# Performance work log

Measured on AMD Instinct MI355X. Metric: run time of the kernel, lower is better.

Reference implementation:

```python
import jax, jax.numpy as jnp
import numpy as np

B, C, H, W = 32, 256, 7, 7
HEADS = 8
DIM_HEAD = 64
INNER = HEADS * DIM_HEAD  # 512
N_ANGLES = 16
KS = 5
GROUPS = 32
EPS = 1e-5


def setup_inputs() -> dict:
    key = jax.random.key(0)
    ks = jax.random.split(key, 16)
    w = lambda k, shp: jax.random.normal(k, shp, jnp.float32) * 0.05
    return {
        'x': jax.random.normal(ks[0], (B, C, H, W), jnp.float32),
        'gn_g': jnp.ones((C,), jnp.float32), 'gn_b': jnp.zeros((C,), jnp.float32),
        'sa_w1': w(ks[1], (C // 8, C)), 'sa_b1': jnp.zeros((C // 8,), jnp.float32),
        'sa_w2': w(ks[2], (C, C // 8)), 'sa_b2': jnp.zeros((C,), jnp.float32),
        'sa_gn_g': jnp.ones((C,), jnp.float32), 'sa_gn_b': jnp.zeros((C,), jnp.float32),
        'ra_gn_g': jnp.ones((C,), jnp.float32), 'ra_gn_b': jnp.zeros((C,), jnp.float32),
        'ra_qkv_w': w(ks[3], (3 * C, C)),
        'ra_proj_w': w(ks[4], (C, C)), 'ra_proj_b': jnp.zeros((C,), jnp.float32),
        'aa_ln_g': jnp.ones((C,), jnp.float32), 'aa_ln_b': jnp.zeros((C,), jnp.float32),
        'aa_qkv_w': w(ks[5], (3 * INNER, C)),
        'aa_relpos': w(ks[6], (2 * 7 - 1, 2 * 7 - 1, HEADS)),
        'aa_out_w': w(ks[7], (C, INNER)), 'aa_out_b': jnp.zeros((C,), jnp.float32),
        'ad_dir_w': w(ks[8], (N_ANGLES, C, C, KS, KS)),
        'ad_ap_w1': w(ks[9], (128, C)), 'ad_ap_b1': jnp.zeros((128,), jnp.float32),
        'ad_ap_w2': w(ks[10], (N_ANGLES, 128)), 'ad_ap_b2': jnp.zeros((N_ANGLES,), jnp.float32),
        'ad_proj_w': w(ks[11], (C, C)), 'ad_proj_b': jnp.zeros((C,), jnp.float32),
        'gate_w': w(ks[12], (4, C)), 'gate_b': jnp.zeros((4,), jnp.float32),
        'proj_w': w(ks[13], (C, C)), 'proj_b': jnp.zeros((C,), jnp.float32),
    }


def _gn(x, g, b):
    Bx, Cx, Hx, Wx = x.shape
    xr = x.reshape(Bx, GROUPS, -1)
    m = xr.mean(-1, keepdims=True)
    v = xr.var(-1, keepdims=True)
    xn = ((xr - m) * jax.lax.rsqrt(v + EPS)).reshape(Bx, Cx, Hx, Wx)
    return xn * g[None, :, None, None] + b[None, :, None, None]


def _c1(x, w, b=None):
    y = jnp.einsum('bchw,oc->bohw', x, w)
    return y if b is None else y + b[None, :, None, None]


def _rot_attn_pass(x, qkv_w):
    Bx, Cx, Hx, Wx = x.shape
    d = Cx // HEADS
    q, k, v = jnp.split(_c1(x, qkv_w), 3, axis=1)
    sh = lambda t: t.reshape(Bx, HEADS, d, Hx * Wx).transpose(0, 1, 3, 2)  # b h n d
    q, k, v = sh(q), sh(k), sh(v)
    a = jax.nn.softmax(jnp.einsum('bhid,bhjd->bhij', q, k) * (d ** -0.5), axis=-1)
    o = jnp.einsum('bhij,bhjd->bhid', a, v)
    return o.transpose(0, 1, 3, 2).reshape(Bx, Cx, Hx, Wx)


def _forward(x, gn_g, gn_b, sa_w1, sa_b1, sa_w2, sa_b2, sa_gn_g, sa_gn_b,
             ra_gn_g, ra_gn_b, ra_qkv_w, ra_proj_w, ra_proj_b,
             aa_ln_g, aa_ln_b, aa_qkv_w, aa_relpos, aa_out_w, aa_out_b,
             ad_dir_w, ad_ap_w1, ad_ap_b1, ad_ap_w2, ad_ap_b2, ad_proj_w, ad_proj_b,
             gate_w, gate_b, proj_w, proj_b):
    normed = _gn(x, gn_g, gn_b)

    # --- SpatialAttention branch ---
    wts = jax.nn.sigmoid(_c1(jax.nn.relu(_c1(normed, sa_w1, sa_b1)), sa_w2, sa_b2))
    spatial = _gn(normed * wts + normed, sa_gn_g, sa_gn_b)

    # --- RotationAwareAttention branch: 4 rot90 passes, max-fused ---
    xr = _gn(normed, ra_gn_g, ra_gn_b)
    r0 = _rot_attn_pass(xr, ra_qkv_w)
    r1 = jnp.rot90(_rot_attn_pass(jnp.rot90(xr, 1, (2, 3)), ra_qkv_w), 3, (2, 3))
    r2 = jnp.rot90(_rot_attn_pass(jnp.rot90(xr, 2, (2, 3)), ra_qkv_w), 2, (2, 3))
    r3 = jnp.rot90(_rot_attn_pass(jnp.rot90(xr, 3, (2, 3)), ra_qkv_w), 1, (2, 3))
    mx = jnp.maximum(jnp.maximum(r0, r1), jnp.maximum(r2, r3))
    rotation = _c1(mx, ra_proj_w, ra_proj_b) + normed

    # --- AngleAwareSelfAttention branch (rel-pos-biased MHSA over 49 tokens) ---
    Nn = H * W
    t = normed.reshape(B, C, Nn).transpose(0, 2, 1)  # [B,N,C]
    mu = t.mean(-1, keepdims=True)
    var = t.var(-1, keepdims=True)
    tn = (t - mu) * jax.lax.rsqrt(var + EPS) * aa_ln_g + aa_ln_b
    q, k, v = jnp.split(jnp.einsum('bnc,oc->bno', tn, aa_qkv_w), 3, axis=-1)
    sh = lambda u: u.reshape(B, Nn, HEADS, DIM_HEAD).transpose(0, 2, 1, 3)
    q, k, v = sh(q), sh(k), sh(v)
    dots = jnp.einsum('bhid,bhjd->bhij', q, k) * (DIM_HEAD ** -0.5)
    idx = jnp.arange(Nn)
    yi, xi = idx // W, idx % W
    dy = yi[None, :] - yi[:, None] + (H - 1)  # offsets into 13x13 table
    dx = xi[None, :] - xi[:, None] + (W - 1)
    bias = aa_relpos[dy, dx].transpose(2, 0, 1)[None]  # [1,heads,N,N]
    attn = jax.nn.softmax(dots + bias, axis=-1)
    o = jnp.einsum('bhij,bhjd->bhid', attn, v).transpose(0, 2, 1, 3).reshape(B, Nn, INNER)
    o = jnp.einsum('bni,oi->bno', o, aa_out_w) + aa_out_b
    angle = o.transpose(0, 2, 1).reshape(B, C, H, W) + normed

    # --- AngleAdaptiveAttention branch: 16 directional 5x5 convs + learned softmax gate ---
    dir_out = jax.lax.conv_general_dilated(
        normed, ad_dir_w.reshape(N_ANGLES * C, C, KS, KS), (1, 1), 'SAME',
        dimension_numbers=('NCHW', 'OIHW', 'NCHW')).reshape(B, N_ANGLES, C, H, W)
    gap = normed.mean((2, 3))  # [B,C]
    h1 = jax.nn.relu(gap @ ad_ap_w1.T + ad_ap_b1)
    aw = jax.nn.softmax(h1 @ ad_ap_w2.T + ad_ap_b2, axis=1)  # [B,16]
    comb = jnp.einsum('bkchw,bk->bchw', dir_out, aw)
    adaptive = _c1(comb, ad_proj_w, ad_proj_b) + normed

    # --- gated fusion ---
    gates = jax.nn.softmax(_c1(x, gate_w, gate_b), axis=1)  # [B,4,H,W]
    fused = (spatial * gates[:, 0:1] + rotation * gates[:, 1:2]
             + angle * gates[:, 2:3] + adaptive * gates[:, 3:4])
    return _c1(fused, proj_w, proj_b) + x


def reference(x, gn_g, gn_b, sa_w1, sa_b1, sa_w2, sa_b2, sa_gn_g, sa_gn_b,
              ra_gn_g, ra_gn_b, ra_qkv_w, ra_proj_w, ra_proj_b,
              aa_ln_g, aa_ln_b, aa_qkv_w, aa_relpos, aa_out_w, aa_out_b,
              ad_dir_w, ad_ap_w1, ad_ap_b1, ad_ap_w2, ad_ap_b2, ad_proj_w, ad_proj_b,
              gate_w, gate_b, proj_w, proj_b):
    return _forward(x, gn_g, gn_b, sa_w1, sa_b1, sa_w2, sa_b2, sa_gn_g, sa_gn_b,
                    ra_gn_g, ra_gn_b, ra_qkv_w, ra_proj_w, ra_proj_b,
                    aa_ln_g, aa_ln_b, aa_qkv_w, aa_relpos, aa_out_w, aa_out_b,
                    ad_dir_w, ad_ap_w1, ad_ap_b1, ad_ap_w2, ad_ap_b2, ad_proj_w, ad_proj_b,
                    gate_w, gate_b, proj_w, proj_b)
```

## Files before the change

kernel.cpp:

```cpp
#include <hip/hip_runtime.h>

#define EPS 1e-5f
typedef unsigned short u16;
typedef unsigned int u32;
typedef float f32x4 __attribute__((ext_vector_type(4)));
typedef short bf16x8 __attribute__((ext_vector_type(8)));
typedef unsigned int u32x2 __attribute__((ext_vector_type(2)));

__device__ __forceinline__ float bf2f(u16 h){
  return __uint_as_float(((u32)h) << 16);
}
__device__ __forceinline__ u16 f2bf(float f){
  u32 u = __float_as_uint(f);
  u += 0x7fffu + ((u >> 16) & 1u);
  return (u16)(u >> 16);
}
__device__ __forceinline__ u32 pk2(float lo, float hi){
  return ((u32)f2bf(hi) << 16) | (u32)f2bf(lo);
}
union BF8 { bf16x8 v; u32 u[4]; };

__global__ __launch_bounds__(256) void k_prep1(
    const float* __restrict__ x, const float* __restrict__ gn_g, const float* __restrict__ gn_b,
    const float* __restrict__ ra_g, const float* __restrict__ ra_b,
    float* __restrict__ normed, float* __restrict__ xr, float* __restrict__ gap)
{
  int ch = blockIdx.x, b = blockIdx.y;
  int c0 = ch * 32;
  __shared__ float xs[1568], ns[1568];
  const float* xb = x + ((size_t)b * 256 + c0) * 49;
  for (int i = threadIdx.x; i < 1568; i += 256) xs[i] = xb[i];
  __syncthreads();
  int wv = threadIdx.x >> 6, lane = threadIdx.x & 63;
  const float* gsrc = xs + wv * 392;
  float* ndst = ns + wv * 392;
  float s = 0.f, ss = 0.f;
  for (int i = lane; i < 392; i += 64){ float v = gsrc[i]; s += v; ss += v * v; }
  for (int off = 32; off; off >>= 1){ s += __shfl_down(s, off); ss += __shfl_down(ss, off); }
  s = __shfl(s, 0); ss = __shfl(ss, 0);
  float m = s / 392.f, rs = rsqrtf(ss / 392.f - m * m + EPS);
  for (int i = lane; i < 392; i += 64){
    int c = c0 + wv * 8 + i / 49;
    ndst[i] = (gsrc[i] - m) * rs * gn_g[c] + gn_b[c];
  }
  __syncthreads();
  float* nb = normed + ((size_t)b * 256 + c0) * 49;
  for (int i = threadIdx.x; i < 1568; i += 256) nb[i] = ns[i];
  if (threadIdx.x < 32){
    float g2 = 0.f; const float* rp = ns + threadIdx.x * 49;
    for (int p = 0; p < 49; p++) g2 += rp[p];
    gap[(size_t)b * 256 + c0 + threadIdx.x] = g2 * (1.f / 49.f);
  }
  s = 0.f; ss = 0.f;
  for (int i = lane; i < 392; i += 64){ float v = ndst[i]; s += v; ss += v * v; }
  for (int off = 32; off; off >>= 1){ s += __shfl_down(s, off); ss += __shfl_down(ss, off); }
  s = __shfl(s, 0); ss = __shfl(ss, 0);
  m = s / 392.f; rs = rsqrtf(ss / 392.f - m * m + EPS);
  float* xrb = xr + ((size_t)b * 256 + c0) * 49;
  for (int i = lane; i < 392; i += 64){
    int c = c0 + wv * 8 + i / 49;
    xrb[wv * 392 + i] = (ndst[i] - m) * rs * ra_g[c] + ra_b[c];
  }
}

__device__ void dev_pos(
    const float* __restrict__ x, const float* __restrict__ normed,
    const float* __restrict__ gate_w, const float* __restrict__ gate_b,
    float* __restrict__ gates_g, float* __restrict__ lnm_g, float* __restrict__ lnr_g,
    int pc, int b, float* sm)
{
  float* gw = sm;
  for (int i = threadIdx.x; i < 1024; i += 256) gw[i] = gate_w[i];
  __syncthreads();
  int wv = threadIdx.x >> 6, lane = threadIdx.x & 63;
  for (int pi = wv; pi < 7; pi += 4){
    int p = pc * 7 + pi;
    const float* nb = normed + (size_t)b * 12544 + p;
    const float* xb = x + (size_t)b * 12544 + p;
    float s = 0.f, ss = 0.f, g0 = 0.f, g1 = 0.f, g2 = 0.f, g3 = 0.f;
    for (int c = lane; c < 256; c += 64){
      float nv = nb[c * 49];
      float xv = xb[c * 49];
      s += nv; ss += nv * nv;
      g0 += xv * gw[c]; g1 += xv * gw[256 + c];
      g2 += xv * gw[512 + c]; g3 += xv * gw[768 + c];
    }
    for (int off = 32; off; off >>= 1){
      s += __shfl_down(s, off); ss += __shfl_down(ss, off);
      g0 += __shfl_down(g0, off); g1 += __shfl_down(g1, off);
      g2 += __shfl_down(g2, off); g3 += __shfl_down(g3, off);
    }
    if (lane == 0){
      float mu = s / 256.f;
      lnm_g[b * 49 + p] = mu;
      lnr_g[b * 49 + p] = rsqrtf(ss / 256.f - mu * mu + EPS);
      g0 += gate_b[0]; g1 += gate_b[1]; g2 += gate_b[2]; g3 += gate_b[3];
      float mx = fmaxf(fmaxf(g0, g1), fmaxf(g2, g3));
      float e0 = __expf(g0 - mx), e1 = __expf(g1 - mx), e2 = __expf(g2 - mx), e3 = __expf(g3 - mx);
      float inv = 1.f / (e0 + e1 + e2 + e3);
      float* gg = gates_g + (size_t)b * 196 + p;
      gg[0] = e0 * inv; gg[49] = e1 * inv; gg[98] = e2 * inv; gg[147] = e3 * inv;
    }
  }
}

__device__ void dev_h1aw(
    const float* __restrict__ normed, const float* __restrict__ sa_w1, const float* __restrict__ sa_b1,
    const float* __restrict__ ap_w1, const float* __restrict__ ap_b1,
    const float* __restrict__ ap_w2, const float* __restrict__ ap_b2,
    const float* __restrict__ gap_g,
    float* __restrict__ h1_g, float* __restrict__ aw_g,
    int xb2, int b, float* sm)
{
  int t = threadIdx.x;
  if (xb2 == 7){
    float* gaps = sm; float* h = sm + 256; float* lg = sm + 384;
    gaps[t] = gap_g[b * 256 + t];
    __syncthreads();
    if (t < 128){
      float s = ap_b1[t];
      const float* wr = ap_w1 + t * 256;
      #pragma unroll 4
      for (int c = 0; c < 256; c++) s += gaps[c] * wr[c];
      h[t] = fmaxf(s, 0.f);
    }
    __syncthreads();
    if (t < 16){
      float s = ap_b2[t];
      const float* wr = ap_w2 + t * 128;
      #pragma unroll 4
      for (int o = 0; o < 128; o++) s += h[o] * wr[o];
      lg[t] = s;
    }
    __syncthreads();
    if (t == 0){
      float mx = -1e30f;
      for (int k = 0; k < 16; k++) mx = fmaxf(mx, lg[k]);
      float e[16], smm = 0.f;
      for (int k = 0; k < 16; k++){ e[k] = __expf(lg[k] - mx); smm += e[k]; }
      float inv = 1.f / smm;
      for (int k = 0; k < 16; k++) aw_g[b * 16 + k] = e[k] * inv;
    }
    return;
  }
  float* w1t = sm;
  float* ns2 = sm + 8448;
  int p0 = xb2 * 7;
  for (int i = t; i < 8192; i += 256){
    int o = i >> 8, c = i & 255;
    w1t[c * 33 + o] = sa_w1[i];
  }
  for (int i = t; i < 1792; i += 256){
    int c = i / 7, pl = i - c * 7;
    ns2[i] = normed[(size_t)b * 12544 + c * 49 + p0 + pl];
  }
  __syncthreads();
  if (t < 224){
    int pl = t >> 5, o = t & 31;
    float s = sa_b1[o];
    #pragma unroll 8
    for (int c = 0; c < 256; c++) s += ns2[c * 7 + pl] * w1t[c * 33 + o];
    h1_g[(size_t)b * 1568 + (p0 + pl) * 32 + o] = fmaxf(s, 0.f);
  }
}

__global__ __launch_bounds__(256) void k_pre2(
    const float* __restrict__ x, const float* __restrict__ normed,
    const float* __restrict__ gate_w, const float* __restrict__ gate_b,
    const float* __restrict__ sa_w1, const float* __restrict__ sa_b1,
    const float* __restrict__ ap_w1, const float* __restrict__ ap_b1,
    const float* __restrict__ ap_w2, const float* __restrict__ ap_b2,
    const float* __restrict__ gap_g,
    float* __restrict__ gates_g, float* __restrict__ lnm_g, float* __restrict__ lnr_g,
    float* __restrict__ h1_g, float* __restrict__ aw_g)
{
  __shared__ float sm[10240];
  int bx = blockIdx.x, b = blockIdx.y;
  if (bx < 7)
    dev_pos(x, normed, gate_w, gate_b, gates_g, lnm_g, lnr_g, bx, b, sm);
  else
    dev_h1aw(normed, sa_w1, sa_b1, ap_w1, ap_b1, ap_w2, ap_b2, gap_g, h1_g, aw_g, bx - 7, b, sm);
}

__device__ void dev_spatial(
    const float* __restrict__ normed, const float* __restrict__ h1_g,
    const float* __restrict__ sa_w2, const float* __restrict__ sa_b2,
    const float* __restrict__ sa_g, const float* __restrict__ sa_bb,
    float* __restrict__ spat_g, int gc, int b, float* sm)
{
  float* h1s = sm;
  float* w2s = sm + 1617;
  int t = threadIdx.x;
  for (int i = t; i < 1568; i += 256){
    int p = i >> 5, o = i & 31;
    h1s[p * 33 + o] = h1_g[(size_t)b * 1568 + i];
  }
  for (int i = t; i < 1024; i += 256) w2s[i] = sa_w2[gc * 1024 + i];
  __syncthreads();
  int wv = t >> 6, lane = t & 63;
  int cg0 = wv * 8;
  const float* nb = normed + (size_t)b * 12544 + (gc * 32 + cg0) * 49;
  float tmp[7];
  float s = 0.f, ss = 0.f;
  #pragma unroll
  for (int j = 0; j < 7; j++){
    int i = lane + 64 * j;
    float v = 0.f;
    if (i < 392){
      int c = i / 49;
      const float* wr = w2s + (cg0 + c) * 32;
      const float* hp = h1s + (i - c * 49) * 33;
      float d = sa_b2[gc * 32 + cg0 + c];
      #pragma unroll
      for (int o = 0; o < 32; o++) d += hp[o] * wr[o];
      v = nb[i] * (1.f + 1.f / (1.f + __expf(-d)));
      s += v; ss += v * v;
    }
    tmp[j] = v;
  }
  for (int off = 32; off; off >>= 1){ s += __shfl_down(s, off); ss += __shfl_down(ss, off); }
  s = __shfl(s, 0); ss = __shfl(ss, 0);
  float m = s / 392.f, rs = rsqrtf(ss / 392.f - m * m + EPS);
  float* sb = spat_g + (size_t)b * 12544 + (gc * 32 + cg0) * 49;
  #pragma unroll
  for (int j = 0; j < 7; j++){
    int i = lane + 64 * j;
    if (i < 392){
      int c = gc * 32 + cg0 + i / 49;
      sb[i] = (tmp[j] - m) * rs * sa_g[c] + sa_bb[c];
    }
  }
}

__device__ void dev_weff(
    const float* __restrict__ W, const float* __restrict__ aw, u16* __restrict__ weff, int bx)
{
  const size_t t = ((size_t)bx * 256 + threadIdx.x) * 4;
  float4 A[16];
  #pragma unroll
  for (int k = 0; k < 16; k++) A[k] = *(const float4*)(W + (size_t)k * 1638400 + t);
  #pragma unroll 1
  for (int b = 0; b < 32; b++){
    float s0 = 0.f, s1 = 0.f, s2 = 0.f, s3 = 0.f;
    #pragma unroll
    for (int k = 0; k < 16; k++){
      float a = aw[b * 16 + k];
      s0 += a * A[k].x; s1 += a * A[k].y; s2 += a * A[k].z; s3 += a * A[k].w;
    }
    u32x2 o; o.x = pk2(s0, s1); o.y = pk2(s2, s3);
    __builtin_nontemporal_store(o, (u32x2*)(weff + (size_t)b * 1638400 + t));
  }
}

__device__ void dev_im2col(
    const float* __restrict__ normed, u16* __restrict__ xim, int p, int b, float* sm)
{
  u16* row = (u16*)sm;
  int ci = threadIdx.x;
  int py = p / 7, px = p - py * 7;
  const float* nb = normed + (size_t)b * 12544 + ci * 49;
  u16* rp = row + ci * 25;
  #pragma unroll
  for (int sy = 0; sy < 5; sy++){
    int iy = py + sy - 2;
    #pragma unroll
    for (int sx = 0; sx < 5; sx++){
      int ix = px + sx - 2;
      float v = (iy >= 0 && iy < 7 && ix >= 0 && ix < 7) ? nb[iy * 7 + ix] : 0.f;
      rp[sy * 5 + sx] = f2bf(v);
    }
  }
  __syncthreads();
  const u32* rs = (const u32*)row;
  u32* od = (u32*)(xim + (size_t)(b * 49 + p) * 6400);
  for (int i = threadIdx.x; i < 3200; i += 256) od[i] = rs[i];
}

__device__ __forceinline__ void mfma_gemm_dev(
    const float* __restrict__ W, const float* __restrict__ bias,
    const float* __restrict__ act, const float* __restrict__ res,
    float* __restrict__ out, int M, int K, int m0blk, int p0, int b,
    const float* __restrict__ lnm, const float* __restrict__ lnr,
    const float* __restrict__ lng, const float* __restrict__ lnb)
{
  int wv = threadIdx.x >> 6, lane = threadIdx.x & 63;
  int lo = lane & 15, hi = lane >> 4;
  int m0 = m0blk + wv * 32;
  int p = p0 + lo;
  bool pok = p < 49;
  const float* ab = act + (size_t)b * K * 49;
  float lm = 0.f, lr = 0.f;
  if (lng && pok){ lm = lnm[p]; lr = lnr[p]; }
  f32x4 acc0 = {0.f, 0.f, 0.f, 0.f};
  f32x4 acc1 = {0.f, 0.f, 0.f, 0.f};
  const float* wr0 = W + (size_t)(m0 + lo) * K + hi * 8;
  const float* wr1 = W + (size_t)(m0 + 16 + lo) * K + hi * 8;
  for (int k0 = 0; k0 < K; k0 += 32){
    int kb = k0 + hi * 8;
    float4 a0lo = *(const float4*)(wr0 + k0);
    float4 a0hi = *(const float4*)(wr0 + k0 + 4);
    float4 a1lo = *(const float4*)(wr1 + k0);
    float4 a1hi = *(const float4*)(wr1 + k0 + 4);
    float bv[8];
    if (pok){
      const float* ap = ab + (size_t)kb * 49 + p;
      #pragma unroll
      for (int i = 0; i < 8; i++) bv[i] = ap[i * 49];
      if (lng){
        #pragma unroll
        for (int i = 0; i < 8; i++) bv[i] = (bv[i] - lm) * lr * lng[kb + i] + lnb[kb + i];
      }
    } else {
      #pragma unroll
      for (int i = 0; i < 8; i++) bv[i] = 0.f;
    }
    BF8 A0, A1, B;
    A0.u[0] = pk2(a0lo.x, a0lo.y); A0.u[1] = pk2(a0lo.z, a0lo.w);
    A0.u[2] = pk2(a0hi.x, a0hi.y); A0.u[3] = pk2(a0hi.z, a0hi.w);
    A1.u[0] = pk2(a1lo.x, a1lo.y); A1.u[1] = pk2(a1lo.z, a1lo.w);
    A1.u[2] = pk2(a1hi.x, a1hi.y); A1.u[3] = pk2(a1hi.z, a1hi.w);
    B.u[0] = pk2(bv[0], bv[1]); B.u[1] = pk2(bv[2], bv[3]);
    B.u[2] = pk2(bv[4], bv[5]); B.u[3] = pk2(bv[6], bv[7]);
    acc0 = __builtin_amdgcn_mfma_f32_16x16x32_bf16(A0.v, B.v, acc0, 0, 0, 0);
    acc1 = __builtin_amdgcn_mfma_f32_16x16x32_bf16(A1.v, B.v, acc1, 0, 0, 0);
  }
  if (pok){
    #pragma unroll
    for (int r = 0; r < 4; r++){
      int m = m0 + hi * 4 + r;
      size_t idx = ((size_t)b * M + m) * 49 + p;
      float v = acc0[r] + (bias ? bias[m] : 0.f);
      if (res) v += res[idx];
      out[idx] = v;
      int m2 = m + 16;
      size_t idx2 = idx + 16 * 49;
      float v2 = acc1[r] + (bias ? bias[m2] : 0.f);
      if (res) v2 += res[idx2];
      out[idx2] = v2;
    }
  }
}

__global__ __launch_bounds__(256) void k_mega1(
    const float* __restrict__ ad_dir_w, const float* __restrict__ aw, u16* __restrict__ weff,
    const float* __restrict__ ra_w, const float* __restrict__ aa_w,
    const float* __restrict__ xr, const float* __restrict__ normed,
    const float* __restrict__ lnm, const float* __restrict__ lnr,
    const float* __restrict__ ln_g, const float* __restrict__ ln_b,
    float* __restrict__ ra_qkv, float* __restrict__ aa_qkv,
    u16* __restrict__ xim,
    const float* __restrict__ h1_g, const float* __restrict__ sa_w2, const float* __restrict__ sa_b2,
    const float* __restrict__ sa_g, const float* __restrict__ sa_bb, float* __restrict__ spat_g)
{
  __shared__ float sm[3300];
  int id = (blockIdx.x * 2003) % 5728;
  if (id < 1600){
    dev_weff(ad_dir_w, aw, weff, id);
  } else if (id < 3904){
    int q = id - 1600;
    int bx = q % 72, b = q / 72;
    if (bx < 24){
      int m0 = (bx >> 2) * 128, p0 = (bx & 3) * 16;
      mfma_gemm_dev(ra_w, nullptr, xr, nullptr, ra_qkv, 768, 256, m0, p0, b,
                    nullptr, nullptr, nullptr, nullptr);
    } else {
      int bx2 = bx - 24;
      int m0 = (bx2 >> 2) * 128, p0 = (bx2 & 3) * 16;
      mfma_gemm_dev(aa_w, nullptr, normed, nullptr, aa_qkv, 1536, 256, m0, p0, b,
                    lnm + b * 49, lnr + b * 49, ln_g, ln_b);
    }
  } else if (id < 5472){
    int q = id - 3904;
    dev_im2col(normed, xim, q % 49, q / 49, sm);
  } else {
    int q = id - 5472;
    dev_spatial(normed, h1_g, sa_w2, sa_b2, sa_g, sa_bb, spat_g, q % 8, q / 8, sm);
  }
}

__device__ void dev_conv(
    const u16* __restrict__ weff, const u16* __restrict__ xim, float* __restrict__ partial,
    int bx, int b)
{
  int mblk = bx >> 3, kp = bx & 7;
  int wv = threadIdx.x >> 6, lane = threadIdx.x & 63;
  int lo = lane & 15, hi = lane >> 4;
  int co0 = mblk * 128 + wv * 32;
  const u16* wr0 = weff + (size_t)b * 1638400 + (size_t)(co0 + lo) * 6400 + kp * 800 + hi * 8;
  const u16* wr1 = wr0 + 16 * 6400;
  const u16* xb = xim + (size_t)b * 313600 + (size_t)lo * 6400 + kp * 800 + hi * 8;
  f32x4 acc[2][4];
  #pragma unroll
  for (int mi = 0; mi < 2; mi++)
    #pragma unroll
    for (int pi = 0; pi < 4; pi++) acc[mi][pi] = (f32x4){0.f, 0.f, 0.f, 0.f};
  #pragma unroll 1
  for (int ks = 0; ks < 25; ks++){
    int k0 = ks * 32;
    bf16x8 A0 = __builtin_nontemporal_load((const bf16x8*)(wr0 + k0));
    bf16x8 A1 = __builtin_nontemporal_load((const bf16x8*)(wr1 + k0));
    bf16x8 B0 = *(const bf16x8*)(xb + k0);
    bf16x8 B1 = *(const bf16x8*)(xb + 16 * 6400 + k0);
    bf16x8 B2 = *(const bf16x8*)(xb + 32 * 6400 + k0);
    bf16x8 B3 = *(const bf16x8*)(xb + 48 * 6400 + k0);
    acc[0][0] = __builtin_amdgcn_mfma_f32_16x16x32_bf16(A0, B0, acc[0][0], 0, 0, 0);
    acc[0][1] = __builtin_amdgcn_mfma_f32_16x16x32_bf16(A0, B1, acc[0][1], 0, 0, 0);
    acc[0][2] = __builtin_amdgcn_mfma_f32_16x16x32_bf16(A0, B2, acc[0][2], 0, 0, 0);
    acc[0][3] = __builtin_amdgcn_mfma_f32_16x16x32_bf16(A0, B3, acc[0][3], 0, 0, 0);
    acc[1][0] = __builtin_amdgcn_mfma_f32_16x16x32_bf16(A1, B0, acc[1][0], 0, 0, 0);
    acc[1][1] = __builtin_amdgcn_mfma_f32_16x16x32_bf16(A1, B1, acc[1][1], 0, 0, 0);
    acc[1][2] = __builtin_amdgcn_mfma_f32_16x16x32_bf16(A1, B2, acc[1][2], 0, 0, 0);
    acc[1][3] = __builtin_amdgcn_mfma_f32_16x16x32_bf16(A1, B3, acc[1][3], 0, 0, 0);
  }
  float* pb = partial + ((size_t)kp * 32 + b) * 12544;
  #pragma unroll
  for (int mi = 0; mi < 2; mi++){
    #pragma unroll
    for (int pi = 0; pi < 4; pi++){
      int p = pi * 16 + lo;
      if (p < 49){
        #pragma unroll
        for (int r = 0; r < 4; r++){
          int co = co0 + mi * 16 + hi * 4 + r;
          pb[co * 49 + p] = acc[mi][pi][r];
        }
      }
    }
  }
}

__device__ __forceinline__ void softmax_rows(float* sc, int tid)
{
  int r = tid >> 2, q = tid & 3;
  if (r < 49){
    float* row = sc + r * 52;
    float mx = -1e30f;
    for (int j = q; j < 49; j += 4) mx = fmaxf(mx, row[j]);
    mx = fmaxf(mx, __shfl_xor(mx, 1));
    mx = fmaxf(mx, __shfl_xor(mx, 2));
    float sm = 0.f;
    for (int j = q; j < 49; j += 4){ float e = __expf(row[j] - mx); row[j] = e; sm += e; }
    sm += __shfl_xor(sm, 1);
    sm += __shfl_xor(sm, 2);
    float inv = 1.f / sm;
    for (int j = q; j < 49; j += 4) row[j] *= inv;
  }
}

__device__ void dev_attn(
    const float* __restrict__ ra_qkv, const float* __restrict__ aa_qkv,
    const float* __restrict__ relpos,
    float* __restrict__ r0, float* __restrict__ ao,
    int xb2, int b, float* sm)
{
  if (xb2 < 8){
    int hd = xb2;
    float* qs = sm; float* ks = sm + 1617; float* vs = sm + 3234; float* sc = sm + 4851;
    const float* base = ra_qkv + (size_t)b * 768 * 49;
    for (int i = threadIdx.x; i < 1568; i += 256){
      int d = i / 49, tok = i - d * 49;
      qs[tok * 33 + d] = base[(hd * 32 + d) * 49 + tok];
      ks[tok * 33 + d] = base[(256 + hd * 32 + d) * 49 + tok];
      vs[tok * 33 + d] = base[(512 + hd * 32 + d) * 49 + tok];
    }
    __syncthreads();
    const float scale = 0.17677669529663687f;
    for (int it = threadIdx.x; it < 2401; it += 256){
      int i = it / 49, j = it - i * 49;
      float s = 0.f;
      #pragma unroll
      for (int d = 0; d < 32; d++) s += qs[i * 33 + d] * ks[j * 33 + d];
      sc[i * 52 + j] = s * scale;
    }
    __syncthreads();
    softmax_rows(sc, threadIdx.x);
    __syncthreads();
    for (int it = threadIdx.x; it < 1568; it += 256){
      int d = it / 49, i = it - d * 49;
      float o = 0.f;
      for (int j = 0; j < 49; j++) o += sc[i * 52 + j] * vs[j * 33 + d];
      r0[((size_t)b * 256 + hd * 32 + d) * 49 + i] = o;
    }
  } else {
    int hd = xb2 - 8;
    float* qs = sm; float* ks = sm + 3185; float* vs = sm + 6370; float* sc = sm + 9555;
    const float* base = aa_qkv + (size_t)b * 1536 * 49;
    for (int i = threadIdx.x; i < 3136; i += 256){
      int d = i / 49, tok = i - d * 49;
      qs[tok * 65 + d] = base[(hd * 64 + d) * 49 + tok];
      ks[tok * 65 + d] = base[(512 + hd * 64 + d) * 49 + tok];
      vs[tok * 65 + d] = base[(1024 + hd * 64 + d) * 49 + tok];
    }
    __syncthreads();
    for (int it = threadIdx.x; it < 2401; it += 256){
      int i = it / 49, j = it - i * 49;
      float s = 0.f;
      #pragma unroll
      for (int d = 0; d < 64; d++) s += qs[i * 65 + d] * ks[j * 65 + d];
      int dy = j / 7 - i / 7 + 6, dx = j % 7 - i % 7 + 6;
      sc[i * 52 + j] = s * 0.125f + relpos[(dy * 13 + dx) * 8 + hd];
    }
    __syncthreads();
    softmax_rows(sc, threadIdx.x);
    __syncthreads();
    for (int it = threadIdx.x; it < 3136; it += 256){
      int d = it / 49, i = it - d * 49;
      float o = 0.f;
      for (int j = 0; j < 49; j++) o += sc[i * 52 + j] * vs[j * 65 + d];
      ao[((size_t)b * 512 + hd * 64 + d) * 49 + i] = o;
    }
  }
}

__global__ __launch_bounds__(256) void k_mega2(
    const u16* __restrict__ weff, const u16* __restrict__ xim, float* __restrict__ partial,
    const float* __restrict__ ra_qkv, const float* __restrict__ aa_qkv,
    const float* __restrict__ relpos, float* __restrict__ r0, float* __restrict__ ao)
{
  __shared__ float sm[12103];
  int id = blockIdx.x;
  int q = id >> 1;
  if ((id & 1) == 0){
    dev_conv(weff, xim, partial, q % 16, q / 16);
  } else {
    dev_attn(ra_qkv, aa_qkv, relpos, r0, ao, q % 16, q / 16, sm);
  }
}

__global__ __launch_bounds__(256) void k_conv_reduce(
    const float* __restrict__ part, float* __restrict__ comb)
{
  int i = blockIdx.x * 256 + threadIdx.x;
  if (i >= 100352) return;
  float a0 = 0.f, a1 = 0.f, a2 = 0.f, a3 = 0.f;
  #pragma unroll
  for (int p = 0; p < 8; p++){
    float4 v = ((const float4*)part)[(size_t)p * 100352 + i];
    a0 += v.x; a1 += v.y; a2 += v.z; a3 += v.w;
  }
  float4 o; o.x = a0; o.y = a1; o.z = a2; o.w = a3;
  ((float4*)comb)[i] = o;
}

__global__ __launch_bounds__(256) void k_proj3(
    const float* __restrict__ ra_pw, const float* __restrict__ ra_pb, const float* __restrict__ r0,
    const float* __restrict__ aa_ow, const float* __restrict__ aa_ob, const float* __restrict__ aa_o,
    const float* __restrict__ ad_pw, const float* __restrict__ ad_pb, const float* __restrict__ comb,
    const float* __restrict__ normed,
    float* __restrict__ rotf, float* __restrict__ angf, float* __restrict__ adpf)
{
  int bx = blockIdx.x, b = blockIdx.y;
  if (bx < 8){
    int m0 = (bx >> 2) * 128, p0 = (bx & 3) * 16;
    mfma_gemm_dev(ra_pw, ra_pb, r0, normed, rotf, 256, 256, m0, p0, b,
                  nullptr, nullptr, nullptr, nullptr);
  } else if (bx < 16){
    int bx2 = bx - 8;
    int m0 = (bx2 >> 2) * 128, p0 = (bx2 & 3) * 16;
    mfma_gemm_dev(aa_ow, aa_ob, aa_o, normed, angf, 256, 512, m0, p0, b,
                  nullptr, nullptr, nullptr, nullptr);
  } else {
    int bx2 = bx - 16;
    int m0 = (bx2 >> 2) * 128, p0 = (bx2 & 3) * 16;
    mfma_gemm_dev(ad_pw, ad_pb, comb, normed, adpf, 256, 256, m0, p0, b,
                  nullptr, nullptr, nullptr, nullptr);
  }
}

__global__ __launch_bounds__(256) void k_final(
    const float* __restrict__ proj_w, const float* __restrict__ proj_b,
    const float* __restrict__ spat, const float* __restrict__ rotf,
    const float* __restrict__ angf, const float* __restrict__ adpf,
    const float* __restrict__ gates, const float* __restrict__ x,
    float* __restrict__ out)
{
  int bx = blockIdx.x, b = blockIdx.y;
  int wv = threadIdx.x >> 6, lane = threadIdx.x & 63;
  int lo = lane & 15, hi = lane >> 4;
  int m0 = (bx >> 2) * 128 + wv * 32;
  int p0 = (bx & 3) * 16;
  int p = p0 + lo;
  bool pok = p < 49;
  float g0 = 0.f, g1 = 0.f, g2 = 0.f, g3 = 0.f;
  if (pok){
    const float* g = gates + (size_t)b * 196 + p;
    g0 = g[0]; g1 = g[49]; g2 = g[98]; g3 = g[147];
  }
  size_t boff = (size_t)b * 12544;
  f32x4 acc0 = {0.f, 0.f, 0.f, 0.f};
  f32x4 acc1 = {0.f, 0.f, 0.f, 0.f};
  const float* wr0 = proj_w + (size_t)(m0 + lo) * 256 + hi * 8;
  const float* wr1 = wr0 + 16 * 256;
  for (int k0 = 0; k0 < 256; k0 += 32){
    int kb = k0 + hi * 8;
    float4 a0lo = *(const float4*)(wr0 + k0);
    float4 a0hi = *(const float4*)(wr0 + k0 + 4);
    float4 a1lo = *(const float4*)(wr1 + k0);
    float4 a1hi = *(const float4*)(wr1 + k0 + 4);
    float bv[8];
    if (pok){
      size_t base = boff + (size_t)kb * 49 + p;
      #pragma unroll
      for (int i = 0; i < 8; i++){
        size_t idx = base + (size_t)i * 49;
        bv[i] = spat[idx] * g0 + rotf[idx] * g1 + angf[idx] * g2 + adpf[idx] * g3;
      }
    } else {
      #pragma unroll
      for (int i = 0; i < 8; i++) bv[i] = 0.f;
    }
    BF8 A0, A1, B;
    A0.u[0] = pk2(a0lo.x, a0lo.y); A0.u[1] = pk2(a0lo.z, a0lo.w);
    A0.u[2] = pk2(a0hi.x, a0hi.y); A0.u[3] = pk2(a0hi.z, a0hi.w);
    A1.u[0] = pk2(a1lo.x, a1lo.y); A1.u[1] = pk2(a1lo.z, a1lo.w);
    A1.u[2] = pk2(a1hi.x, a1hi.y); A1.u[3] = pk2(a1hi.z, a1hi.w);
    B.u[0] = pk2(bv[0], bv[1]); B.u[1] = pk2(bv[2], bv[3]);
    B.u[2] = pk2(bv[4], bv[5]); B.u[3] = pk2(bv[6], bv[7]);
    acc0 = __builtin_amdgcn_mfma_f32_16x16x32_bf16(A0.v, B.v, acc0, 0, 0, 0);
    acc1 = __builtin_amdgcn_mfma_f32_16x16x32_bf16(A1.v, B.v, acc1, 0, 0, 0);
  }
  if (pok){
    #pragma unroll
    for (int r = 0; r < 4; r++){
      int m = m0 + hi * 4 + r;
      size_t idx = boff + (size_t)m * 49 + p;
      out[idx] = acc0[r] + proj_b[m] + x[idx];
      int m2 = m + 16;
      size_t idx2 = idx + 16 * 49;
      out[idx2] = acc1[r] + proj_b[m2] + x[idx2];
    }
  }
}

extern "C" void kernel_launch(void* const* d_in, const int* in_sizes, int n_in,
                              void* d_out, int out_size, void* d_ws, size_t ws_size,
                              hipStream_t stream)
{
  const float* x        = (const float*)d_in[0];
  const float* gn_g     = (const float*)d_in[1];
  const float* gn_b     = (const float*)d_in[2];
  const float* sa_w1    = (const float*)d_in[3];
  const float* sa_b1    = (const float*)d_in[4];
  const float* sa_w2    = (const float*)d_in[5];
  const float* sa_b2    = (const float*)d_in[6];
  const float* sa_gn_g  = (const float*)d_in[7];
  const float* sa_gn_b  = (const float*)d_in[8];
  const float* ra_gn_g  = (const float*)d_in[9];
  const float* ra_gn_b  = (const float*)d_in[10];
  const float* ra_qkv_w = (const float*)d_in[11];
  const float* ra_proj_w= (const float*)d_in[12];
  const float* ra_proj_b= (const float*)d_in[13];
  const float* aa_ln_g  = (const float*)d_in[14];
  const float* aa_ln_b  = (const float*)d_in[15];
  const float* aa_qkv_w = (const float*)d_in[16];
  const float* aa_relpos= (const float*)d_in[17];
  const float* aa_out_w = (const float*)d_in[18];
  const float* aa_out_b = (const float*)d_in[19];
  const float* ad_dir_w = (const float*)d_in[20];
  const float* ad_ap_w1 = (const float*)d_in[21];
  const float* ad_ap_b1 = (const float*)d_in[22];
  const float* ad_ap_w2 = (const float*)d_in[23];
  const float* ad_ap_b2 = (const float*)d_in[24];
  const float* ad_proj_w= (const float*)d_in[25];
  const float* ad_proj_b= (const float*)d_in[26];
  const float* gate_w   = (const float*)d_in[27];
  const float* gate_b   = (const float*)d_in[28];
  const float* proj_w   = (const float*)d_in[29];
  const float* proj_b   = (const float*)d_in[30];

  char* ws = (char*)d_ws;
  float* normed    = (float*)(ws + 0);
  float* xr        = (float*)(ws + 1605632);
  float* h1_g      = (float*)(ws + 3211264);
  float* lnm       = (float*)(ws + 3420160);
  float* lnr       = (float*)(ws + 3426560);
  float* spatial   = (float*)(ws + 4816896);
  float* rotf      = (float*)(ws + 6422528);
  float* anglef    = (float*)(ws + 8028160);
  float* adaptf    = (float*)(ws + 9633792);
  float* r0        = (float*)(ws + 12845056);
  float* gap       = (float*)(ws + 14450688);
  float* aw        = (float*)(ws + 14483456);
  float* gates     = (float*)(ws + 14485504);
  float* ra_qkv    = (float*)(ws + 14510592);
  float* aa_qkv    = (float*)(ws + 19327488);
  float* aa_o      = (float*)(ws + 28961280);
  float* comb      = (float*)(ws + 32172544);
  float* partial   = (float*)(ws + 33778176);
  u16*   xim       = (u16*)  (ws + 46623232);
  u16*   weff      = (u16*)  (ws + 66693632);

  float* out = (float*)d_out;

  k_prep1<<<dim3(8, 32), 256, 0, stream>>>(x, gn_g, gn_b, ra_gn_g, ra_gn_b, normed, xr, gap);
  k_pre2<<<dim3(15, 32), 256, 0, stream>>>(x, normed, gate_w, gate_b,
                                           sa_w1, sa_b1, ad_ap_w1, ad_ap_b1, ad_ap_w2, ad_ap_b2,
                                           gap, gates, lnm, lnr, h1_g, aw);
  k_mega1<<<dim3(5728), 256, 0, stream>>>(ad_dir_w, aw, weff,
                                          ra_qkv_w, aa_qkv_w, xr, normed,
                                          lnm, lnr, aa_ln_g, aa_ln_b, ra_qkv, aa_qkv,
                                          xim,
                                          h1_g, sa_w2, sa_b2, sa_gn_g, sa_gn_b, spatial);
  k_mega2<<<dim3(1024), 256, 0, stream>>>(weff, xim, partial,
                                          ra_qkv, aa_qkv, aa_relpos, r0, aa_o);
  k_conv_reduce<<<dim3(392), 256, 0, stream>>>(partial, comb);
  k_proj3<<<dim3(24, 32), 256, 0, stream>>>(ra_proj_w, ra_proj_b, r0,
                                            aa_out_w, aa_out_b, aa_o,
                                            ad_proj_w, ad_proj_b, comb,
                                            normed, rotf, anglef, adaptf);
  k_final<<<dim3(8, 32), 256, 0, stream>>>(proj_w, proj_b, spatial, rotf, anglef, adaptf,
                                           gates, x, out);
}
```

Before: 250.2 us.

## Split effective-weight build and conv into halves staggered across mega kernels

The effective directional-weight build is split in two. Half is computed in k_mega1 and the other half in k_mega2, alongside the conv for the first output-channel block and the attention work. The second conv block moves into a new k_mega3 together with the rotation and angle projections, leaving only the adaptive projection in its own kernel. The aim is to balance work across launches and overlap the heavy weight generation with independent work, which shortens per-kernel tails. It relies on the first 800 weff blocks covering exactly the channels used by conv block 0, and it adds an extra launch.

```diff
diff --git a/kernel.cpp b/kernel.cpp
--- a/kernel.cpp
+++ b/kernel.cpp
@@ -341,43 +341,6 @@
   }
 }
 
-__global__ __launch_bounds__(256) void k_mega1(
-    const float* __restrict__ ad_dir_w, const float* __restrict__ aw, u16* __restrict__ weff,
-    const float* __restrict__ ra_w, const float* __restrict__ aa_w,
-    const float* __restrict__ xr, const float* __restrict__ normed,
-    const float* __restrict__ lnm, const float* __restrict__ lnr,
-    const float* __restrict__ ln_g, const float* __restrict__ ln_b,
-    float* __restrict__ ra_qkv, float* __restrict__ aa_qkv,
-    u16* __restrict__ xim,
-    const float* __restrict__ h1_g, const float* __restrict__ sa_w2, const float* __restrict__ sa_b2,
-    const float* __restrict__ sa_g, const float* __restrict__ sa_bb, float* __restrict__ spat_g)
-{
-  __shared__ float sm[3300];
-  int id = (blockIdx.x * 2003) % 5728;
-  if (id < 1600){
-    dev_weff(ad_dir_w, aw, weff, id);
-  } else if (id < 3904){
-    int q = id - 1600;
-    int bx = q % 72, b = q / 72;
-    if (bx < 24){
-      int m0 = (bx >> 2) * 128, p0 = (bx & 3) * 16;
-      mfma_gemm_dev(ra_w, nullptr, xr, nullptr, ra_qkv, 768, 256, m0, p0, b,
-                    nullptr, nullptr, nullptr, nullptr);
-    } else {
-      int bx2 = bx - 24;
-      int m0 = (bx2 >> 2) * 128, p0 = (bx2 & 3) * 16;
-      mfma_gemm_dev(aa_w, nullptr, normed, nullptr, aa_qkv, 1536, 256, m0, p0, b,
-                    lnm + b * 49, lnr + b * 49, ln_g, ln_b);
-    }
-  } else if (id < 5472){
-    int q = id - 3904;
-    dev_im2col(normed, xim, q % 49, q / 49, sm);
-  } else {
-    int q = id - 5472;
-    dev_spatial(normed, h1_g, sa_w2, sa_b2, sa_g, sa_bb, spat_g, q % 8, q / 8, sm);
-  }
-}
-
 __device__ void dev_conv(
     const u16* __restrict__ weff, const u16* __restrict__ xim, float* __restrict__ partial,
     int bx, int b)
@@ -512,18 +475,85 @@
   }
 }
 
+__global__ __launch_bounds__(256) void k_mega1(
+    const float* __restrict__ ad_dir_w, const float* __restrict__ aw, u16* __restrict__ weff,
+    const float* __restrict__ ra_w, const float* __restrict__ aa_w,
+    const float* __restrict__ xr, const float* __restrict__ normed,
+    const float* __restrict__ lnm, const float* __restrict__ lnr,
+    const float* __restrict__ ln_g, const float* __restrict__ ln_b,
+    float* __restrict__ ra_qkv, float* __restrict__ aa_qkv,
+    u16* __restrict__ xim,
+    const float* __restrict__ h1_g, const float* __restrict__ sa_w2, const float* __restrict__ sa_b2,
+    const float* __restrict__ sa_g, const float* __restrict__ sa_bb, float* __restrict__ spat_g)
+{
+  __shared__ float sm[3300];
+  int id = (int)(((long long)blockIdx.x * 2003) % 4928);
+  if (id < 800){
+    dev_weff(ad_dir_w, aw, weff, id);
+  } else if (id < 3104){
+    int q = id - 800;
+    int bx = q % 72, b = q / 72;
+    if (bx < 24){
+      int m0 = (bx >> 2) * 128, p0 = (bx & 3) * 16;
+      mfma_gemm_dev(ra_w, nullptr, xr, nullptr, ra_qkv, 768, 256, m0, p0, b,
+                    nullptr, nullptr, nullptr, nullptr);
+    } else {
+      int bx2 = bx - 24;
+      int m0 = (bx2 >> 2) * 128, p0 = (bx2 & 3) * 16;
+      mfma_gemm_dev(aa_w, nullptr, normed, nullptr, aa_qkv, 1536, 256, m0, p0, b,
+                    lnm + b * 49, lnr + b * 49, ln_g, ln_b);
+    }
+  } else if (id < 4672){
+    int q = id - 3104;
+    dev_im2col(normed, xim, q % 49, q / 49, sm);
+  } else {
+    int q = id - 4672;
+    dev_spatial(normed, h1_g, sa_w2, sa_b2, sa_g, sa_bb, spat_g, q % 8, q / 8, sm);
+  }
+}
+
 __global__ __launch_bounds__(256) void k_mega2(
-    const u16* __restrict__ weff, const u16* __restrict__ xim, float* __restrict__ partial,
+    const float* __restrict__ ad_dir_w, const float* __restrict__ aw, u16* __restrict__ weff,
+    const u16* __restrict__ xim, float* __restrict__ partial,
     const float* __restrict__ ra_qkv, const float* __restrict__ aa_qkv,
     const float* __restrict__ relpos, float* __restrict__ r0, float* __restrict__ ao)
 {
   __shared__ float sm[12103];
-  int id = blockIdx.x;
-  int q = id >> 1;
-  if ((id & 1) == 0){
-    dev_conv(weff, xim, partial, q % 16, q / 16);
+  int id = (int)(((long long)blockIdx.x * 1051) % 1568);
+  if (id < 800){
+    dev_weff(ad_dir_w, aw, weff, id + 800);
+  } else if (id < 1056){
+    int q = id - 800;
+    dev_conv(weff, xim, partial, q & 7, q >> 3);
   } else {
+    int q = id - 1056;
     dev_attn(ra_qkv, aa_qkv, relpos, r0, ao, q % 16, q / 16, sm);
+  }
+}
+
+__global__ __launch_bounds__(256) void k_mega3(
+    const u16* __restrict__ weff, const u16* __restrict__ xim, float* __restrict__ partial,
+    const float* __restrict__ ra_pw, const float* __restrict__ ra_pb, const float* __restrict__ r0,
+    const float* __restrict__ aa_ow, const float* __restrict__ aa_ob, const float* __restrict__ aa_o,
+    const float* __restrict__ normed,
+    float* __restrict__ rotf, float* __restrict__ angf)
+{
+  int id = (int)(((long long)blockIdx.x * 389) % 768);
+  if (id < 256){
+    dev_conv(weff, xim, partial, 8 + (id & 7), id >> 3);
+  } else {
+    int q = id - 256;
+    int sub = q % 16, b = q / 16;
+    if (sub < 8){
+      int m0 = (sub >> 2) * 128, p0 = (sub & 3) * 16;
+      mfma_gemm_dev(ra_pw, ra_pb, r0, normed, rotf, 256, 256, m0, p0, b,
+                    nullptr, nullptr, nullptr, nullptr);
+    } else {
+      int s2 = sub - 8;
+      int m0 = (s2 >> 2) * 128, p0 = (s2 & 3) * 16;
+      mfma_gemm_dev(aa_ow, aa_ob, aa_o, normed, angf, 256, 512, m0, p0, b,
+                    nullptr, nullptr, nullptr, nullptr);
+    }
   }
 }
 
@@ -542,29 +572,15 @@
   ((float4*)comb)[i] = o;
 }
 
-__global__ __launch_bounds__(256) void k_proj3(
-    const float* __restrict__ ra_pw, const float* __restrict__ ra_pb, const float* __restrict__ r0,
-    const float* __restrict__ aa_ow, const float* __restrict__ aa_ob, const float* __restrict__ aa_o,
-    const float* __restrict__ ad_pw, const float* __restrict__ ad_pb, const float* __restrict__ comb,
-    const float* __restrict__ normed,
-    float* __restrict__ rotf, float* __restrict__ angf, float* __restrict__ adpf)
+__global__ __launch_bounds__(256) void k_proj_ad(
+    const float* __restrict__ ad_pw, const float* __restrict__ ad_pb,
+    const float* __restrict__ comb, const float* __restrict__ normed,
+    float* __restrict__ adpf)
 {
   int bx = blockIdx.x, b = blockIdx.y;
-  if (bx < 8){
-    int m0 = (bx >> 2) * 128, p0 = (bx & 3) * 16;
-    mfma_gemm_dev(ra_pw, ra_pb, r0, normed, rotf, 256, 256, m0, p0, b,
-                  nullptr, nullptr, nullptr, nullptr);
-  } else if (bx < 16){
-    int bx2 = bx - 8;
-    int m0 = (bx2 >> 2) * 128, p0 = (bx2 & 3) * 16;
-    mfma_gemm_dev(aa_ow, aa_ob, aa_o, normed, angf, 256, 512, m0, p0, b,
-                  nullptr, nullptr, nullptr, nullptr);
-  } else {
-    int bx2 = bx - 16;
-    int m0 = (bx2 >> 2) * 128, p0 = (bx2 & 3) * 16;
-    mfma_gemm_dev(ad_pw, ad_pb, comb, normed, adpf, 256, 256, m0, p0, b,
-                  nullptr, nullptr, nullptr, nullptr);
-  }
+  int m0 = (bx >> 2) * 128, p0 = (bx & 3) * 16;
+  mfma_gemm_dev(ad_pw, ad_pb, comb, normed, adpf, 256, 256, m0, p0, b,
+                nullptr, nullptr, nullptr, nullptr);
 }
 
 __global__ __launch_bounds__(256) void k_final(
@@ -696,18 +712,19 @@
   k_pre2<<<dim3(15, 32), 256, 0, stream>>>(x, normed, gate_w, gate_b,
                                            sa_w1, sa_b1, ad_ap_w1, ad_ap_b1, ad_ap_w2, ad_ap_b2,
                                            gap, gates, lnm, lnr, h1_g, aw);
-  k_mega1<<<dim3(5728), 256, 0, stream>>>(ad_dir_w, aw, weff,
+  k_mega1<<<dim3(4928), 256, 0, stream>>>(ad_dir_w, aw, weff,
                                           ra_qkv_w, aa_qkv_w, xr, normed,
                                           lnm, lnr, aa_ln_g, aa_ln_b, ra_qkv, aa_qkv,
                                           xim,
                                           h1_g, sa_w2, sa_b2, sa_gn_g, sa_gn_b, spatial);
-  k_mega2<<<dim3(1024), 256, 0, stream>>>(weff, xim, partial,
+  k_mega2<<<dim3(1568), 256, 0, stream>>>(ad_dir_w, aw, weff, xim, partial,
                                           ra_qkv, aa_qkv, aa_relpos, r0, aa_o);
+  k_mega3<<<dim3(768), 256, 0, stream>>>(weff, xim, partial,
+                                         ra_proj_w, ra_proj_b, r0,
+                                         aa_out_w, aa_out_b, aa_o,
+                                         normed, rotf, anglef);
   k_conv_reduce<<<dim3(392), 256, 0, stream>>>(partial, comb);
-  k_proj3<<<dim3(24, 32), 256, 0, stream>>>(ra_proj_w, ra_proj_b, r0,
-                                            aa_out_w, aa_out_b, aa_o,
-                                            ad_proj_w, ad_proj_b, comb,
-                                            normed, rotf, anglef, adaptf);
+  k_proj_ad<<<dim3(8, 32), 256, 0, stream>>>(ad_proj_w, ad_proj_b, comb, normed, adaptf);
   k_final<<<dim3(8, 32), 256, 0, stream>>>(proj_w, proj_b, spatial, rotf, anglef, adaptf,
                                            gates, x, out);
 }
```

Measured after the change: 275.8 us. +10.2%, slower.
